# Kernel optimization log

Hardware: AMD Instinct MI355X
Metric: run time of the kernel (lower is better)

The kernel has to match this reference:

```python
import jax, jax.numpy as jnp
import numpy as np

S = 4096      # keystrokes
H = 32        # hidden_dim / d_model
NH = 8        # nhead
HD = H // NH  # head dim = 4
FF = 2048     # torch TransformerEncoderLayer default dim_feedforward
NL = 6        # num_layers
EPS = 1e-5


def setup_inputs() -> dict:
    key = jax.random.key(0)
    ks = jax.random.split(key, 20)
    sc = 0.02
    ts = jnp.sort(jax.random.uniform(ks[0], (S,), minval=0.0, maxval=2.49e7))
    feats = jax.random.normal(ks[1], (S, 2), dtype=jnp.float32)
    data = jnp.concatenate([ts[:, None], feats], axis=1)  # [S, 3]
    return {
        "data": data,
        "lin_w": jax.random.normal(ks[2], (H, 2)) * sc,
        "lin_b": jnp.zeros((H,)),
        "qkv_w": jax.random.normal(ks[3], (NL, 3 * H, H)) * sc,
        "qkv_b": jnp.zeros((NL, 3 * H)),
        "out_w": jax.random.normal(ks[4], (NL, H, H)) * sc,
        "out_b": jnp.zeros((NL, H)),
        "ln1_g": jnp.ones((NL, H)),
        "ln1_b": jnp.zeros((NL, H)),
        "ff1_w": jax.random.normal(ks[5], (NL, FF, H)) * sc,
        "ff1_b": jnp.zeros((NL, FF)),
        "ff2_w": jax.random.normal(ks[6], (NL, H, FF)) * sc,
        "ff2_b": jnp.zeros((NL, H)),
        "ln2_g": jnp.ones((NL, H)),
        "ln2_b": jnp.zeros((NL, H)),
        "cls_w": jax.random.normal(ks[7], (1, H)) * sc,
        "cls_b": jnp.zeros((1,)),
    }


def _ln(x, g, b):
    m = x.mean(-1, keepdims=True)
    v = ((x - m) ** 2).mean(-1, keepdims=True)
    return (x - m) / jnp.sqrt(v + EPS) * g + b


def reference(data, lin_w, lin_b, qkv_w, qkv_b, out_w, out_b,
              ln1_g, ln1_b, ff1_w, ff1_b, ff2_w, ff2_b,
              ln2_g, ln2_b, cls_w, cls_b):
    # per-keystroke Linear+ReLU, vectorized over the sequence
    x = jax.nn.relu(data[:, 1:] @ lin_w.T + lin_b)            # [S, H]
    # sinusoidal time encoding at index timestamp//100
    ts_idx = (data[:, 0] / 100.0).astype(jnp.int32)            # [S]
    div = jnp.exp(jnp.arange(0, H, 2, dtype=jnp.float32) * (-np.log(10000.0) / H))
    ang = ts_idx[:, None].astype(jnp.float32) * div            # [S, H/2]
    pe = jnp.stack([jnp.sin(ang), jnp.cos(ang)], axis=-1).reshape(S, H)
    x = x + pe
    # prepend CLS token of -1.0 -> seq len S+1
    x = jnp.concatenate([jnp.full((1, H), -1.0, dtype=x.dtype), x], axis=0)
    L = S + 1
    for i in range(NL):  # post-LN encoder layers (torch defaults, eval/no-dropout)
        qkv = x @ qkv_w[i].T + qkv_b[i]                        # [L, 3H]
        q, k, v = jnp.split(qkv, 3, axis=-1)
        q = q.reshape(L, NH, HD)
        k = k.reshape(L, NH, HD)
        v = v.reshape(L, NH, HD)
        scores = jnp.einsum('qhd,khd->hqk', q, k) / np.sqrt(HD)
        attn = jax.nn.softmax(scores, axis=-1)                 # [NH, L, L]
        o = jnp.einsum('hqk,khd->qhd', attn, v).reshape(L, H)
        o = o @ out_w[i].T + out_b[i]
        x = _ln(x + o, ln1_g[i], ln1_b[i])
        f = jax.nn.relu(x @ ff1_w[i].T + ff1_b[i]) @ ff2_w[i].T + ff2_b[i]
        x = _ln(x + f, ln2_g[i], ln2_b[i])
    cls_out = x[0]                                             # [H]
    return jax.nn.sigmoid(cls_out @ cls_w.T + cls_b)           # [1]
```

## Files before the change

kernel.cpp:

```cpp
#include <hip/hip_runtime.h>
#include <hip/hip_bf16.h>
#include <math.h>

#define SEQ 4096
#define LL  4097
#define HDIM 32
#define FFD 2048
#define NLAYER 6
#define EPSLN 1e-5f
#define NCHUNK 16
#define KPAD 4128
#define QROWS 4352
#define XROWS 4160
#define RT 64
#define FS 128
#define NSEG 8

#if __has_builtin(__builtin_amdgcn_exp2f)
#define EXP2 __builtin_amdgcn_exp2f
#else
#define EXP2 exp2f
#endif

#define QSCALE 0.7213475204444817f

typedef short bf16x8 __attribute__((ext_vector_type(8)));
typedef short bf16x4 __attribute__((ext_vector_type(4)));
typedef float f32x4 __attribute__((ext_vector_type(4)));

__device__ __forceinline__ unsigned short f2b(float f) {
  unsigned int b = __float_as_uint(f);
  b += 0x7FFFu + ((b >> 16) & 1u);
  return (unsigned short)(b >> 16);
}

__device__ __forceinline__ unsigned int pk_bf16(float a, float b) {
  __hip_bfloat162 h = __float22bfloat162_rn(make_float2(a, b));
  return *(unsigned int*)&h;
}

__device__ __forceinline__ f32x4 mfma_qk(bf16x4 a, bf16x4 b, f32x4 c) {
#if __has_builtin(__builtin_amdgcn_mfma_f32_16x16x16bf16_1k)
  return __builtin_amdgcn_mfma_f32_16x16x16bf16_1k(a, b, c, 0, 0, 0);
#else
  bf16x8 a8 = {a[0], a[1], a[2], a[3], 0, 0, 0, 0};
  bf16x8 b8 = {b[0], b[1], b[2], b[3], 0, 0, 0, 0};
  return __builtin_amdgcn_mfma_f32_16x16x32_bf16(a8, b8, c, 0, 0, 0);
#endif
}


__device__ __forceinline__ void qkv_wave(float y, int row, bool ok, int lane,
    const float* __restrict__ qw, const float* __restrict__ qb,
    unsigned short* __restrict__ Qb, unsigned short* __restrict__ KB4,
    unsigned short* __restrict__ VB5) {
  int ch = lane & 31;
  float xv[32];
#pragma unroll
  for (int k = 0; k < 32; ++k) xv[k] = __shfl(y, (lane & 32) + k, 64);
#pragma unroll
  for (int t3 = 0; t3 < 3; ++t3) {
    int cc = t3 * 32 + ch;
    const float4* wr = (const float4*)(qw + (size_t)cc * 32);
    float acc = qb[cc];
#pragma unroll
    for (int k8 = 0; k8 < 8; ++k8) {
      float4 wv = wr[k8];
      acc = fmaf(xv[4 * k8 + 0], wv.x, acc);
      acc = fmaf(xv[4 * k8 + 1], wv.y, acc);
      acc = fmaf(xv[4 * k8 + 2], wv.z, acc);
      acc = fmaf(xv[4 * k8 + 3], wv.w, acc);
    }
    if (ok) {
      int h = ch >> 2;
      if (t3 == 0) {
        Qb[(size_t)row * 32 + ch] = f2b(QSCALE * acc);
      } else if (t3 == 1) {
        KB4[((size_t)h * KPAD + row) * 4 + (ch & 3)] = f2b(acc);
      } else {
        int w = row & 31;
        int pos = ((w & 15) << 1) | (w >> 4);
        VB5[((size_t)h * 5 + (ch & 3)) * KPAD + (row & ~31) + pos] = f2b(acc);
      }
    }
  }
}

__global__ __launch_bounds__(256) void k_init(const float* __restrict__ data,
    const float* __restrict__ lin_w, const float* __restrict__ lin_b,
    const float* __restrict__ qkv_w, const float* __restrict__ qkv_b,
    const float* __restrict__ ff1_w, const float* __restrict__ ff2_w,
    float* __restrict__ X, unsigned short* __restrict__ Qb,
    unsigned short* __restrict__ KB4, unsigned short* __restrict__ VB5,
    unsigned short* __restrict__ W1B, unsigned short* __restrict__ W2B) {
  int gid = blockIdx.x * 256 + threadIdx.x;
  int gsz = gridDim.x * 256;
  const int NW = NLAYER * FFD * 32;
  for (int i = gid; i < NW; i += gsz) {
    W1B[i] = f2b(ff1_w[i]);
    W2B[i] = f2b(ff2_w[i]);
  }
  for (int i = gid; i < (QROWS - LL) * 32; i += gsz)
    Qb[(size_t)LL * 32 + i] = 0;
  for (int i = gid; i < 8 * (KPAD - LL) * 4; i += gsz) {
    int hh = i / ((KPAD - LL) * 4);
    int rem = i % ((KPAD - LL) * 4);
    KB4[((size_t)hh * KPAD + LL) * 4 + rem] = 0;
  }
  for (int i = gid; i < 8 * 5 * KPAD; i += gsz) {
    int col = i % KPAD;
    int dd = (i / KPAD) % 5;
    if (dd == 4) {
      int key = (col & ~31) + ((col & 1) << 4) + ((col & 31) >> 1);
      VB5[i] = (key <= 4096) ? 0x3F80 : 0;
    } else if (col > 4096) {
      VB5[i] = 0;
    }
  }
  int wave = threadIdx.x >> 6, lane = threadIdx.x & 63;
  int r = lane >> 5, ch = lane & 31;
  unsigned wgid = blockIdx.x * 4 + wave;
  for (unsigned it = wgid; it < 2049; it += gridDim.x * 4) {
    int row = it * 2 + r;
    bool ok = row < LL;
    float val = 0.f;
    if (ok) {
      if (row == 0) {
        val = -1.0f;
      } else {
        int s = row - 1;
        float ts = data[s * 3 + 0];
        float f0 = data[s * 3 + 1];
        float f1 = data[s * 3 + 2];
        float lin = f0 * lin_w[ch * 2 + 0] + f1 * lin_w[ch * 2 + 1] + lin_b[ch];
        lin = fmaxf(lin, 0.0f);
        int tsi = (int)(ts / 100.0f);
        int j = ch >> 1;
        float aj = (float)(2 * j) * (float)(-0.28782313662425575);
        float divj = (float)exp((double)aj);
        float ang = (float)tsi * divj;
        float pe = (ch & 1) ? cosf(ang) : sinf(ang);
        val = lin + pe;
      }
      X[(size_t)row * HDIM + ch] = val;
    }
    qkv_wave(val, row, ok, lane, qkv_w, qkv_b, Qb, KB4, VB5);
  }
}

__global__ __launch_bounds__(256, 4) void k_attn(
    const unsigned short* __restrict__ Qb, const unsigned short* __restrict__ KB4,
    const unsigned short* __restrict__ VB5, float* __restrict__ LP,
    float4* __restrict__ AP4) {
  int tid = threadIdx.x;
  int wave = tid >> 6, lane = tid & 63;
  int l16 = lane & 15, quad = lane >> 4;
  int h = blockIdx.y, c = blockIdx.z;
  int qs = blockIdx.x * 4 + wave;
  if (qs >= 65) return;
  int q0 = qs * 64;
  int kb0 = c * 256;
  int nkb = (c == NCHUNK - 1) ? 9 : 8;

  const unsigned short* KBh = KB4 + (size_t)h * KPAD * 4;
  const unsigned short* VBh = VB5 + (size_t)h * 5 * KPAD;
  const bool kl = (quad == (h & 3));
  const bool vl = (l16 < 5);
  const int qcol0 = (h >> 2) * 16 + quad * 4;

  bf16x4 aq[4];
#pragma unroll
  for (int t = 0; t < 4; ++t)
    aq[t] = *(const bf16x4*)&Qb[(size_t)(q0 + t * 16 + l16) * 32 + qcol0];

  const bf16x4 zb4 = {0, 0, 0, 0};
  const bf16x8 zb8 = {0, 0, 0, 0, 0, 0, 0, 0};
  f32x4 acc0[4], acc1[4];
#pragma unroll
  for (int t = 0; t < 4; ++t) {
    acc0[t] = (f32x4){0.f, 0.f, 0.f, 0.f};
    acc1[t] = (f32x4){0.f, 0.f, 0.f, 0.f};
  }

  auto step = [&](int k0, f32x4* acc) {
    bf16x4 bk0 = kl ? *(const bf16x4*)&KBh[(size_t)(k0 + l16) * 4] : zb4;
    bf16x4 bk1 = kl ? *(const bf16x4*)&KBh[(size_t)(k0 + 16 + l16) * 4] : zb4;
    bf16x8 bv = vl ? *(const bf16x8*)&VBh[(size_t)l16 * KPAD + k0 + quad * 8]
                   : zb8;
    f32x4 z = {0.f, 0.f, 0.f, 0.f};
    unsigned pf[4][4];
#pragma unroll
    for (int t = 0; t < 4; ++t) {
      f32x4 s0 = mfma_qk(bk0, aq[t], z);
      f32x4 s1 = mfma_qk(bk1, aq[t], z);
#pragma unroll
      for (int reg = 0; reg < 4; ++reg)
        pf[t][reg] = pk_bf16(EXP2(s0[reg]), EXP2(s1[reg]));
    }
#pragma unroll
    for (int t = 0; t < 4; ++t) {
      bf16x8 pb = *(const bf16x8*)&pf[t][0];
      acc[t] = __builtin_amdgcn_mfma_f32_16x16x32_bf16(bv, pb, acc[t], 0, 0, 0);
    }
  };

  int kb = 0;
  for (; kb + 2 <= nkb; kb += 2) {
    step(kb0 + kb * 32, acc0);
    step(kb0 + (kb + 1) * 32, acc1);
  }
  if (kb < nkb) step(kb0 + kb * 32, acc0);

#pragma unroll
  for (int t = 0; t < 4; ++t) {
    f32x4 a = acc0[t] + acc1[t];
    int q = q0 + t * 16 + l16;
    if (q < LL) {
      if (quad == 0) {
        AP4[((size_t)c * LL + q) * 8 + h] = make_float4(a[0], a[1], a[2], a[3]);
      } else if (quad == 1) {
        LP[((size_t)c * LL + q) * 8 + h] = a[0];
      }
    }
  }
}

__global__ __launch_bounds__(256) void k_oproj(const float* __restrict__ LP,
    const float* __restrict__ APf, float* __restrict__ x,
    unsigned short* __restrict__ Xb,
    const float* __restrict__ ow, const float* __restrict__ ob,
    const float* __restrict__ g, const float* __restrict__ bln) {
  int tid = threadIdx.x;
  int wave = tid >> 6, lane = tid & 63;
  int r = lane >> 5, ch = lane & 31;
  int row = blockIdx.x * 8 + wave * 2 + r;
  bool ok = row < LL;
  int hh = ch >> 2;
  float L = 0.f, A = 0.f;
  if (ok) {
#pragma unroll
    for (int c = 0; c < NCHUNK; ++c) {
      A += APf[((size_t)c * LL + row) * 32 + ch];
      L += LP[((size_t)c * LL + row) * 8 + hh];
    }
  }
  float os = ok ? A / L : 0.f;
  float acc = 0.f;
  const float4* owr = (const float4*)(ow + (size_t)ch * 32);
#pragma unroll
  for (int k8 = 0; k8 < 8; ++k8) {
    float4 wv = owr[k8];
    acc = fmaf(__shfl(os, (lane & 32) + 4 * k8 + 0, 64), wv.x, acc);
    acc = fmaf(__shfl(os, (lane & 32) + 4 * k8 + 1, 64), wv.y, acc);
    acc = fmaf(__shfl(os, (lane & 32) + 4 * k8 + 2, 64), wv.z, acc);
    acc = fmaf(__shfl(os, (lane & 32) + 4 * k8 + 3, 64), wv.w, acc);
  }
  float val = ok ? (x[(size_t)row * HDIM + ch] + acc + ob[ch]) : 0.f;
  float mean = val;
#pragma unroll
  for (int off = 16; off > 0; off >>= 1) mean += __shfl_xor(mean, off, 32);
  mean *= (1.f / 32.f);
  float d2 = val - mean;
  float var = d2 * d2;
#pragma unroll
  for (int off = 16; off > 0; off >>= 1) var += __shfl_xor(var, off, 32);
  var *= (1.f / 32.f);
  float y = d2 / sqrtf(var + EPSLN) * g[ch] + bln[ch];
  if (ok) {
    x[(size_t)row * HDIM + ch] = y;
    Xb[(size_t)row * HDIM + ch] = f2b(y);
  }
}

__global__ __launch_bounds__(256) void k_ffnA(
    const unsigned short* __restrict__ Xb,
    const unsigned short* __restrict__ w1b, const float* __restrict__ b1,
    const unsigned short* __restrict__ w2b, float* __restrict__ part2) {
  __shared__ unsigned short Fsb[RT * 136];
  int tid = threadIdx.x;
  int r0 = blockIdx.x * RT;
  int wave = tid >> 6, lane = tid & 63;
  int l16 = lane & 15, quad = lane >> 4;
  int m0 = wave * 16;

  bf16x8 a1 = *(const bf16x8*)&Xb[(size_t)(r0 + m0 + l16) * 32 + quad * 8];
  f32x4 acc[2] = {{0.f, 0.f, 0.f, 0.f}, {0.f, 0.f, 0.f, 0.f}};

#pragma unroll
  for (int sg = 0; sg < 2; ++sg) {
    int f0 = (blockIdx.y * 2 + sg) * FS;
    f32x4 c1[8];
#pragma unroll
    for (int t = 0; t < 8; ++t) {
      bf16x8 b =
          *(const bf16x8*)&w1b[(size_t)(f0 + t * 16 + l16) * 32 + quad * 8];
      f32x4 z = {0.f, 0.f, 0.f, 0.f};
      c1[t] = __builtin_amdgcn_mfma_f32_16x16x32_bf16(a1, b, z, 0, 0, 0);
    }
#pragma unroll
    for (int t = 0; t < 8; ++t) {
      float bb = b1[f0 + t * 16 + l16];
#pragma unroll
      for (int reg = 0; reg < 4; ++reg) {
        float v = fmaxf(c1[t][reg] + bb, 0.f);
        int rrow = m0 + quad * 4 + reg;
        Fsb[rrow * 136 + t * 16 + l16] = f2b(v);
      }
    }
#pragma unroll
    for (int kt = 0; kt < 4; ++kt) {
      bf16x8 a2 = *(const bf16x8*)&Fsb[(m0 + l16) * 136 + kt * 32 + quad * 8];
#pragma unroll
      for (int u = 0; u < 2; ++u) {
        bf16x8 b = *(const bf16x8*)&w2b[(size_t)(u * 16 + l16) * FFD + f0 +
                                        kt * 32 + quad * 8];
        acc[u] = __builtin_amdgcn_mfma_f32_16x16x32_bf16(a2, b, acc[u], 0, 0, 0);
      }
    }
  }
#pragma unroll
  for (int u = 0; u < 2; ++u) {
#pragma unroll
    for (int reg = 0; reg < 4; ++reg) {
      int rrow = r0 + m0 + quad * 4 + reg;
      if (rrow < LL)
        part2[((size_t)blockIdx.y * LL + rrow) * HDIM + u * 16 + l16] =
            acc[u][reg];
    }
  }
}

__global__ __launch_bounds__(256) void k_ffnB_qkv(float* __restrict__ x,
    const float* __restrict__ part2, const float* __restrict__ b2,
    const float* __restrict__ g, const float* __restrict__ bln,
    const float* __restrict__ qw, const float* __restrict__ qb,
    unsigned short* __restrict__ Qb, unsigned short* __restrict__ KB4,
    unsigned short* __restrict__ VB5, int do_qkv,
    const float* __restrict__ cw, const float* __restrict__ cb,
    float* __restrict__ out) {
  int tid = threadIdx.x;
  int wave = tid >> 6, lane = tid & 63;
  int r = lane >> 5, ch = lane & 31;
  int row = blockIdx.x * 8 + wave * 2 + r;
  bool ok = row < LL;
  float s = 0.f;
  if (ok) {
#pragma unroll
    for (int q = 0; q < NSEG; ++q)
      s += part2[((size_t)q * LL + row) * HDIM + ch];
  }
  float val = ok ? (x[(size_t)row * HDIM + ch] + s + b2[ch]) : 0.f;
  float mean = val;
#pragma unroll
  for (int off = 16; off > 0; off >>= 1) mean += __shfl_xor(mean, off, 32);
  mean *= (1.f / 32.f);
  float d = val - mean;
  float var = d * d;
#pragma unroll
  for (int off = 16; off > 0; off >>= 1) var += __shfl_xor(var, off, 32);
  var *= (1.f / 32.f);
  float y = d / sqrtf(var + EPSLN) * g[ch] + bln[ch];
  if (ok) x[(size_t)row * HDIM + ch] = y;
  if (!do_qkv) {
    if (blockIdx.x == 0 && wave == 0 && r == 0) {
      float t = y * cw[ch];
#pragma unroll
      for (int off = 16; off > 0; off >>= 1) t += __shfl_xor(t, off, 32);
      if (ch == 0) {
        float z = t + cb[0];
        out[0] = 1.f / (1.f + expf(-z));
      }
    }
    return;
  }
  qkv_wave(y, row, ok, lane, qw, qb, Qb, KB4, VB5);
}

extern "C" void kernel_launch(void* const* d_in, const int* in_sizes, int n_in,
                              void* d_out, int out_size, void* d_ws,
                              size_t ws_size, hipStream_t stream) {
  const float* data  = (const float*)d_in[0];
  const float* lin_w = (const float*)d_in[1];
  const float* lin_b = (const float*)d_in[2];
  const float* qkv_w = (const float*)d_in[3];
  const float* qkv_b = (const float*)d_in[4];
  const float* out_w = (const float*)d_in[5];
  const float* out_b = (const float*)d_in[6];
  const float* ln1_g = (const float*)d_in[7];
  const float* ln1_b = (const float*)d_in[8];
  const float* ff1_w = (const float*)d_in[9];
  const float* ff1_b = (const float*)d_in[10];
  const float* ff2_w = (const float*)d_in[11];
  const float* ff2_b = (const float*)d_in[12];
  const float* ln2_g = (const float*)d_in[13];
  const float* ln2_b = (const float*)d_in[14];
  const float* cls_w = (const float*)d_in[15];
  const float* cls_b = (const float*)d_in[16];

  char* wsb = (char*)d_ws;
  float* X = (float*)wsb;
  unsigned short* Xb  = (unsigned short*)(X + (size_t)LL * 32);
  unsigned short* Qb  = Xb + (size_t)XROWS * 32;
  unsigned short* KB4 = Qb + (size_t)QROWS * 32;
  unsigned short* VB5 = KB4 + (size_t)8 * KPAD * 4;
  unsigned short* W1B = VB5 + (size_t)8 * 5 * KPAD;
  unsigned short* W2B = W1B + (size_t)NLAYER * FFD * 32;
  float4* AP = (float4*)(((size_t)(W2B + (size_t)NLAYER * FFD * 32) + 15) &
                         ~(size_t)15);
  float* LP = (float*)(AP + (size_t)NCHUNK * LL * 8);
  float* PART2 = (float*)AP;

  const int NROWB = (LL + 7) / 8;

  k_init<<<1024, 256, 0, stream>>>(data, lin_w, lin_b, qkv_w, qkv_b,
                                   ff1_w, ff2_w, X, Qb, KB4, VB5, W1B, W2B);
  for (int l = 0; l < NLAYER; ++l) {
    k_attn<<<dim3(17, 8, NCHUNK), 256, 0, stream>>>(Qb, KB4, VB5, LP, AP);
    k_oproj<<<NROWB, 256, 0, stream>>>(
        LP, (const float*)AP, X, Xb, out_w + (size_t)l * 32 * 32,
        out_b + (size_t)l * 32,
        ln1_g + (size_t)l * 32, ln1_b + (size_t)l * 32);
    k_ffnA<<<dim3((LL + RT - 1) / RT, NSEG), 256, 0, stream>>>(
        Xb, W1B + (size_t)l * FFD * 32, ff1_b + (size_t)l * FFD,
        W2B + (size_t)l * FFD * 32, PART2);
    int nl = l + 1;
    int do_qkv = (nl < NLAYER) ? 1 : 0;
    const float* qw = qkv_w + (size_t)(do_qkv ? nl : 0) * 96 * 32;
    const float* qb = qkv_b + (size_t)(do_qkv ? nl : 0) * 96;
    k_ffnB_qkv<<<NROWB, 256, 0, stream>>>(
        X, PART2, ff2_b + (size_t)l * 32,
        ln2_g + (size_t)l * 32, ln2_b + (size_t)l * 32,
        qw, qb, Qb, KB4, VB5, do_qkv, cls_w, cls_b, (float*)d_out);
  }
}
```

Baseline: 437.6 us.

## Fuse out-projection, LayerNorm, FFN and next-layer QKV into one kernel

Merges the out-projection+LN1 kernel, the split FFN kernel and the FFN-reduce+LN2+QKV kernel into a single 512-thread kernel that handles 16 rows per block. Each of the 8 waves covers a 256-wide slice of the feed-forward dimension, and the partial sums are reduced in shared memory rather than through a global partial buffer. This removes two launches per layer and the global round trips for Xb and the FFN partials. In exchange, every block now re-reads the full FF1/FF2 weights for only 16 rows, which cuts weight reuse per block, and the larger shared-memory footprint may limit occupancy.

```diff
diff --git a/kernel.cpp b/kernel.cpp
--- a/kernel.cpp
+++ b/kernel.cpp
@@ -11,10 +11,7 @@
 #define NCHUNK 16
 #define KPAD 4128
 #define QROWS 4352
-#define XROWS 4160
-#define RT 64
-#define FS 128
-#define NSEG 8
+#define RB2 16
 
 #if __has_builtin(__builtin_amdgcn_exp2f)
 #define EXP2 __builtin_amdgcn_exp2f
@@ -225,70 +222,74 @@
   }
 }
 
-__global__ __launch_bounds__(256) void k_oproj(const float* __restrict__ LP,
-    const float* __restrict__ APf, float* __restrict__ x,
-    unsigned short* __restrict__ Xb,
+__global__ __launch_bounds__(512, 4) void k_ffnF(const float* __restrict__ LP,
+    const float* __restrict__ APf, float* __restrict__ X,
     const float* __restrict__ ow, const float* __restrict__ ob,
-    const float* __restrict__ g, const float* __restrict__ bln) {
+    const float* __restrict__ g1, const float* __restrict__ b1ln,
+    const unsigned short* __restrict__ w1b, const float* __restrict__ fb1,
+    const unsigned short* __restrict__ w2b, const float* __restrict__ fb2,
+    const float* __restrict__ g2, const float* __restrict__ b2ln,
+    const float* __restrict__ qw, const float* __restrict__ qb,
+    unsigned short* __restrict__ Qb, unsigned short* __restrict__ KB4,
+    unsigned short* __restrict__ VB5, int do_qkv,
+    const float* __restrict__ cw, const float* __restrict__ cb,
+    float* __restrict__ out) {
+  __shared__ unsigned short Xa[RB2][32];
+  __shared__ float Y1[RB2][32];
+  __shared__ unsigned short Fsb[8][16 * 136];
+  __shared__ float Pr[8][RB2 * 33];
   int tid = threadIdx.x;
   int wave = tid >> 6, lane = tid & 63;
+  int l16 = lane & 15, quad = lane >> 4;
   int r = lane >> 5, ch = lane & 31;
-  int row = blockIdx.x * 8 + wave * 2 + r;
-  bool ok = row < LL;
-  int hh = ch >> 2;
-  float L = 0.f, A = 0.f;
-  if (ok) {
-#pragma unroll
-    for (int c = 0; c < NCHUNK; ++c) {
-      A += APf[((size_t)c * LL + row) * 32 + ch];
-      L += LP[((size_t)c * LL + row) * 8 + hh];
-    }
-  }
-  float os = ok ? A / L : 0.f;
-  float acc = 0.f;
-  const float4* owr = (const float4*)(ow + (size_t)ch * 32);
-#pragma unroll
-  for (int k8 = 0; k8 < 8; ++k8) {
-    float4 wv = owr[k8];
-    acc = fmaf(__shfl(os, (lane & 32) + 4 * k8 + 0, 64), wv.x, acc);
-    acc = fmaf(__shfl(os, (lane & 32) + 4 * k8 + 1, 64), wv.y, acc);
-    acc = fmaf(__shfl(os, (lane & 32) + 4 * k8 + 2, 64), wv.z, acc);
-    acc = fmaf(__shfl(os, (lane & 32) + 4 * k8 + 3, 64), wv.w, acc);
-  }
-  float val = ok ? (x[(size_t)row * HDIM + ch] + acc + ob[ch]) : 0.f;
-  float mean = val;
-#pragma unroll
-  for (int off = 16; off > 0; off >>= 1) mean += __shfl_xor(mean, off, 32);
-  mean *= (1.f / 32.f);
-  float d2 = val - mean;
-  float var = d2 * d2;
-#pragma unroll
-  for (int off = 16; off > 0; off >>= 1) var += __shfl_xor(var, off, 32);
-  var *= (1.f / 32.f);
-  float y = d2 / sqrtf(var + EPSLN) * g[ch] + bln[ch];
-  if (ok) {
-    x[(size_t)row * HDIM + ch] = y;
-    Xb[(size_t)row * HDIM + ch] = f2b(y);
-  }
-}
-
-__global__ __launch_bounds__(256) void k_ffnA(
-    const unsigned short* __restrict__ Xb,
-    const unsigned short* __restrict__ w1b, const float* __restrict__ b1,
-    const unsigned short* __restrict__ w2b, float* __restrict__ part2) {
-  __shared__ unsigned short Fsb[RT * 136];
-  int tid = threadIdx.x;
-  int r0 = blockIdx.x * RT;
-  int wave = tid >> 6, lane = tid & 63;
-  int l16 = lane & 15, quad = lane >> 4;
-  int m0 = wave * 16;
-
-  bf16x8 a1 = *(const bf16x8*)&Xb[(size_t)(r0 + m0 + l16) * 32 + quad * 8];
-  f32x4 acc[2] = {{0.f, 0.f, 0.f, 0.f}, {0.f, 0.f, 0.f, 0.f}};
-
+  int r0 = blockIdx.x * RB2;
+
+  {
+    int rl = wave * 2 + r;
+    int row = r0 + rl;
+    bool ok = row < LL;
+    int hh = ch >> 2;
+    float L = 0.f, A = 0.f;
+    if (ok) {
+#pragma unroll
+      for (int c = 0; c < NCHUNK; ++c) {
+        A += APf[((size_t)c * LL + row) * 32 + ch];
+        L += LP[((size_t)c * LL + row) * 8 + hh];
+      }
+    }
+    float os = ok ? A / L : 0.f;
+    float acc = 0.f;
+    const float4* owr = (const float4*)(ow + (size_t)ch * 32);
+#pragma unroll
+    for (int k8 = 0; k8 < 8; ++k8) {
+      float4 wv = owr[k8];
+      acc = fmaf(__shfl(os, (lane & 32) + 4 * k8 + 0, 64), wv.x, acc);
+      acc = fmaf(__shfl(os, (lane & 32) + 4 * k8 + 1, 64), wv.y, acc);
+      acc = fmaf(__shfl(os, (lane & 32) + 4 * k8 + 2, 64), wv.z, acc);
+      acc = fmaf(__shfl(os, (lane & 32) + 4 * k8 + 3, 64), wv.w, acc);
+    }
+    float val = ok ? (X[(size_t)row * HDIM + ch] + acc + ob[ch]) : 0.f;
+    float mean = val;
+#pragma unroll
+    for (int off = 16; off > 0; off >>= 1) mean += __shfl_xor(mean, off, 32);
+    mean *= (1.f / 32.f);
+    float d2 = val - mean;
+    float var = d2 * d2;
+#pragma unroll
+    for (int off = 16; off > 0; off >>= 1) var += __shfl_xor(var, off, 32);
+    var *= (1.f / 32.f);
+    float y = d2 / sqrtf(var + EPSLN) * g1[ch] + b1ln[ch];
+    Y1[rl][ch] = y;
+    Xa[rl][ch] = ok ? f2b(y) : 0;
+  }
+  __syncthreads();
+
+  bf16x8 a1 = *(const bf16x8*)&Xa[l16][quad * 8];
+  f32x4 acc2[2] = {{0.f, 0.f, 0.f, 0.f}, {0.f, 0.f, 0.f, 0.f}};
+  int fs0 = wave * 256;
 #pragma unroll
   for (int sg = 0; sg < 2; ++sg) {
-    int f0 = (blockIdx.y * 2 + sg) * FS;
+    int f0 = fs0 + sg * 128;
     f32x4 c1[8];
 #pragma unroll
     for (int t = 0; t < 8; ++t) {
@@ -299,81 +300,60 @@
     }
 #pragma unroll
     for (int t = 0; t < 8; ++t) {
-      float bb = b1[f0 + t * 16 + l16];
+      float bb = fb1[f0 + t * 16 + l16];
 #pragma unroll
       for (int reg = 0; reg < 4; ++reg) {
         float v = fmaxf(c1[t][reg] + bb, 0.f);
-        int rrow = m0 + quad * 4 + reg;
-        Fsb[rrow * 136 + t * 16 + l16] = f2b(v);
+        Fsb[wave][(quad * 4 + reg) * 136 + t * 16 + l16] = f2b(v);
       }
     }
 #pragma unroll
     for (int kt = 0; kt < 4; ++kt) {
-      bf16x8 a2 = *(const bf16x8*)&Fsb[(m0 + l16) * 136 + kt * 32 + quad * 8];
+      bf16x8 a2 = *(const bf16x8*)&Fsb[wave][l16 * 136 + kt * 32 + quad * 8];
 #pragma unroll
       for (int u = 0; u < 2; ++u) {
         bf16x8 b = *(const bf16x8*)&w2b[(size_t)(u * 16 + l16) * FFD + f0 +
                                         kt * 32 + quad * 8];
-        acc[u] = __builtin_amdgcn_mfma_f32_16x16x32_bf16(a2, b, acc[u], 0, 0, 0);
-      }
-    }
-  }
-#pragma unroll
-  for (int u = 0; u < 2; ++u) {
-#pragma unroll
-    for (int reg = 0; reg < 4; ++reg) {
-      int rrow = r0 + m0 + quad * 4 + reg;
-      if (rrow < LL)
-        part2[((size_t)blockIdx.y * LL + rrow) * HDIM + u * 16 + l16] =
-            acc[u][reg];
-    }
-  }
-}
-
-__global__ __launch_bounds__(256) void k_ffnB_qkv(float* __restrict__ x,
-    const float* __restrict__ part2, const float* __restrict__ b2,
-    const float* __restrict__ g, const float* __restrict__ bln,
-    const float* __restrict__ qw, const float* __restrict__ qb,
-    unsigned short* __restrict__ Qb, unsigned short* __restrict__ KB4,
-    unsigned short* __restrict__ VB5, int do_qkv,
-    const float* __restrict__ cw, const float* __restrict__ cb,
-    float* __restrict__ out) {
-  int tid = threadIdx.x;
-  int wave = tid >> 6, lane = tid & 63;
-  int r = lane >> 5, ch = lane & 31;
-  int row = blockIdx.x * 8 + wave * 2 + r;
-  bool ok = row < LL;
-  float s = 0.f;
-  if (ok) {
-#pragma unroll
-    for (int q = 0; q < NSEG; ++q)
-      s += part2[((size_t)q * LL + row) * HDIM + ch];
-  }
-  float val = ok ? (x[(size_t)row * HDIM + ch] + s + b2[ch]) : 0.f;
-  float mean = val;
-#pragma unroll
-  for (int off = 16; off > 0; off >>= 1) mean += __shfl_xor(mean, off, 32);
-  mean *= (1.f / 32.f);
-  float d = val - mean;
-  float var = d * d;
-#pragma unroll
-  for (int off = 16; off > 0; off >>= 1) var += __shfl_xor(var, off, 32);
-  var *= (1.f / 32.f);
-  float y = d / sqrtf(var + EPSLN) * g[ch] + bln[ch];
-  if (ok) x[(size_t)row * HDIM + ch] = y;
-  if (!do_qkv) {
-    if (blockIdx.x == 0 && wave == 0 && r == 0) {
+        acc2[u] =
+            __builtin_amdgcn_mfma_f32_16x16x32_bf16(a2, b, acc2[u], 0, 0, 0);
+      }
+    }
+  }
+#pragma unroll
+  for (int u = 0; u < 2; ++u)
+#pragma unroll
+    for (int reg = 0; reg < 4; ++reg)
+      Pr[wave][(quad * 4 + reg) * 33 + u * 16 + l16] = acc2[u][reg];
+  __syncthreads();
+
+  {
+    int rl = wave * 2 + r;
+    int row = r0 + rl;
+    bool ok = row < LL;
+    float s = 0.f;
+#pragma unroll
+    for (int w = 0; w < 8; ++w) s += Pr[w][rl * 33 + ch];
+    float val = ok ? (Y1[rl][ch] + s + fb2[ch]) : 0.f;
+    float mean = val;
+#pragma unroll
+    for (int off = 16; off > 0; off >>= 1) mean += __shfl_xor(mean, off, 32);
+    mean *= (1.f / 32.f);
+    float d2 = val - mean;
+    float var = d2 * d2;
+#pragma unroll
+    for (int off = 16; off > 0; off >>= 1) var += __shfl_xor(var, off, 32);
+    var *= (1.f / 32.f);
+    float y = d2 / sqrtf(var + EPSLN) * g2[ch] + b2ln[ch];
+    if (ok) X[(size_t)row * HDIM + ch] = y;
+    if (do_qkv) {
+      qkv_wave(y, row, ok, lane, qw, qb, Qb, KB4, VB5);
+    } else if (blockIdx.x == 0 && wave == 0 && r == 0) {
       float t = y * cw[ch];
 #pragma unroll
       for (int off = 16; off > 0; off >>= 1) t += __shfl_xor(t, off, 32);
-      if (ch == 0) {
-        float z = t + cb[0];
-        out[0] = 1.f / (1.f + expf(-z));
-      }
-    }
-    return;
-  }
-  qkv_wave(y, row, ok, lane, qw, qb, Qb, KB4, VB5);
+      if (ch == 0) out[0] = 1.f / (1.f + expf(-(t + cb[0])));
+    }
+  }
 }
 
 extern "C" void kernel_launch(void* const* d_in, const int* in_sizes, int n_in,
@@ -399,8 +379,7 @@
 
   char* wsb = (char*)d_ws;
   float* X = (float*)wsb;
-  unsigned short* Xb  = (unsigned short*)(X + (size_t)LL * 32);
-  unsigned short* Qb  = Xb + (size_t)XROWS * 32;
+  unsigned short* Qb  = (unsigned short*)(X + (size_t)LL * 32);
   unsigned short* KB4 = Qb + (size_t)QROWS * 32;
   unsigned short* VB5 = KB4 + (size_t)8 * KPAD * 4;
   unsigned short* W1B = VB5 + (size_t)8 * 5 * KPAD;
@@ -408,27 +387,21 @@
   float4* AP = (float4*)(((size_t)(W2B + (size_t)NLAYER * FFD * 32) + 15) &
                          ~(size_t)15);
   float* LP = (float*)(AP + (size_t)NCHUNK * LL * 8);
-  float* PART2 = (float*)AP;
-
-  const int NROWB = (LL + 7) / 8;
 
   k_init<<<1024, 256, 0, stream>>>(data, lin_w, lin_b, qkv_w, qkv_b,
                                    ff1_w, ff2_w, X, Qb, KB4, VB5, W1B, W2B);
   for (int l = 0; l < NLAYER; ++l) {
     k_attn<<<dim3(17, 8, NCHUNK), 256, 0, stream>>>(Qb, KB4, VB5, LP, AP);
-    k_oproj<<<NROWB, 256, 0, stream>>>(
-        LP, (const float*)AP, X, Xb, out_w + (size_t)l * 32 * 32,
-        out_b + (size_t)l * 32,
-        ln1_g + (size_t)l * 32, ln1_b + (size_t)l * 32);
-    k_ffnA<<<dim3((LL + RT - 1) / RT, NSEG), 256, 0, stream>>>(
-        Xb, W1B + (size_t)l * FFD * 32, ff1_b + (size_t)l * FFD,
-        W2B + (size_t)l * FFD * 32, PART2);
     int nl = l + 1;
     int do_qkv = (nl < NLAYER) ? 1 : 0;
     const float* qw = qkv_w + (size_t)(do_qkv ? nl : 0) * 96 * 32;
     const float* qb = qkv_b + (size_t)(do_qkv ? nl : 0) * 96;
-    k_ffnB_qkv<<<NROWB, 256, 0, stream>>>(
-        X, PART2, ff2_b + (size_t)l * 32,
+    k_ffnF<<<(LL + RB2 - 1) / RB2, 512, 0, stream>>>(
+        LP, (const float*)AP, X,
+        out_w + (size_t)l * 32 * 32, out_b + (size_t)l * 32,
+        ln1_g + (size_t)l * 32, ln1_b + (size_t)l * 32,
+        W1B + (size_t)l * FFD * 32, ff1_b + (size_t)l * FFD,
+        W2B + (size_t)l * FFD * 32, ff2_b + (size_t)l * 32,
         ln2_g + (size_t)l * 32, ln2_b + (size_t)l * 32,
         qw, qb, Qb, KB4, VB5, do_qkv, cls_w, cls_b, (float*)d_out);
   }
```

Result: faster. 400.6 us (-8.4%).
